# Performance work log

Measured on AMD Instinct MI355X. Metric: run time of the kernel, lower is better.

The kernel has to match this reference:

```python
import jax, jax.numpy as jnp
import numpy as np

B, T_IN, D = 16, 512, 256
MAX_DUR = 16


def setup_inputs() -> dict:
    key = jax.random.key(0)
    k1, k2 = jax.random.split(key)
    duration = jax.random.randint(k1, (B, T_IN), 0, MAX_DUR, dtype=jnp.int32)
    encoder_outputs = jax.random.normal(k2, (B, T_IN, D), dtype=jnp.float32)
    mask = jnp.ones((B, T_IN), dtype=bool)
    return {"encoder_outputs": encoder_outputs, "duration": duration, "mask": mask}


def reference(encoder_outputs, duration, mask):
    # duration is a concrete int array here, so T_out is a static Python int
    t_max = int(jnp.max(jnp.sum(duration, axis=-1)))
    d = duration.astype(jnp.float32)
    # frame centers per token: c[b, i] = cumsum(d)[b, i] - 0.5 * d[b, i]
    c = (jnp.cumsum(d, axis=-1) - 0.5 * d)[:, :, None]          # [B, T_in, 1]
    t = jnp.arange(1, t_max + 1, dtype=jnp.float32)[None, None, :]  # [1, 1, T_out]
    w1 = jnp.exp(-0.1 * (t - c) ** 2)                           # [B, T_in, T_out]
    w2 = jnp.sum(w1, axis=1, keepdims=True)                     # [B, 1, T_out]
    w2 = jnp.where(w2 == 0.0, 1.0, w2)
    w = w1 / w2                                                 # [B, T_in, T_out]
    # out[b, t, d] = sum_i w[b, i, t] * enc[b, i, d]
    out = jnp.einsum('bit,bid->btd', w, encoder_outputs)        # [B, T_out, D]
    return (out, w)
```

## Files before the change

kernel.cpp:

```cpp
#include <hip/hip_runtime.h>

#define B_    16
#define T_IN  512
#define D_    256
#define TM    64
#define KI    32
#define AP    40

typedef __attribute__((ext_vector_type(8))) short short8;
typedef __attribute__((ext_vector_type(4))) float f32x4;

__device__ __forceinline__ unsigned short f2bf(float x) {
    unsigned u = __builtin_bit_cast(unsigned, x);
    u += 0x7fff + ((u >> 16) & 1);
    return (unsigned short)(u >> 16);
}

__global__ __launch_bounds__(256) void transpose_kernel(
    const float* __restrict__ enc, unsigned short* __restrict__ encT)
{
    __shared__ float tile[64][65];
    const int tid = threadIdx.x;
    const int b  = blockIdx.z;
    const int i0 = blockIdx.x * 64;
    const int d0 = blockIdx.y * 64;
    #pragma unroll
    for (int p = 0; p < 4; ++p) {
        const int idx = p * 256 + tid;
        const int r   = idx >> 4;
        const int c4  = (idx & 15) * 4;
        const float4 v = *(const float4*)&enc[((long long)b * T_IN + i0 + r) * D_ + d0 + c4];
        tile[r][c4 + 0] = v.x; tile[r][c4 + 1] = v.y;
        tile[r][c4 + 2] = v.z; tile[r][c4 + 3] = v.w;
    }
    __syncthreads();
    #pragma unroll
    for (int p = 0; p < 8; ++p) {
        const int idx = p * 256 + tid;
        const int dr = idx >> 5;
        const int ip = idx & 31;
        const unsigned pk = (unsigned)f2bf(tile[2 * ip][dr])
                          | ((unsigned)f2bf(tile[2 * ip + 1][dr]) << 16);
        *(unsigned*)&encT[((long long)b * D_ + d0 + dr) * T_IN + i0 + ip * 2] = pk;
    }
}

__global__ __launch_bounds__(256, 4) void mfma_kernel(
    const unsigned short* __restrict__ encT,
    const int*   __restrict__ dur,
    float* __restrict__ out,
    int t_out)
{
    __shared__ int   sd[T_IN];
    __shared__ float sc[T_IN];
    __shared__ float red[4][TM];
    __shared__ float sinv[TM];
    __shared__ __align__(16) unsigned short A_lds[2][TM * AP];

    const int tid = threadIdx.x;
    const int b   = blockIdx.y;
    const int t0  = blockIdx.x * TM;

    const int v0 = dur[b * T_IN + tid];
    const int v1 = dur[b * T_IN + tid + 256];
    sd[tid] = v0; sd[tid + 256] = v1;
    __syncthreads();
    for (int off = 1; off < T_IN; off <<= 1) {
        const int a0 = (tid >= off) ? sd[tid - off] : 0;
        const int a1 = sd[tid + 256 - off];
        __syncthreads();
        sd[tid] += a0; sd[tid + 256] += a1;
        __syncthreads();
    }
    sc[tid]       = (float)sd[tid]       - 0.5f * (float)v0;
    sc[tid + 256] = (float)sd[tid + 256] - 0.5f * (float)v1;
    __syncthreads();

    const int tq = tid & 63;
    const int qq = tid >> 6;
    const float tv = (float)(t0 + tq + 1);

    {
        float s = 0.f;
        const int i0 = qq * 128;
        for (int i = 0; i < 128; ++i) {
            const float d = tv - sc[i0 + i];
            s += __expf(-0.1f * d * d);
        }
        red[qq][tq] = s;
        __syncthreads();
        if (qq == 0) {
            const float w2 = red[0][tq] + red[1][tq] + red[2][tq] + red[3][tq];
            sinv[tq] = (w2 == 0.f) ? 1.f : 1.f / w2;
        }
        __syncthreads();
    }

    const int lane  = tid & 63;
    const int mrow  = lane & 15;
    const int quad  = lane >> 4;
    const int dbase = qq * 64;
    const int iq0   = qq * 8;

    f32x4 acc[4][4];
    #pragma unroll
    for (int mf = 0; mf < 4; ++mf)
        #pragma unroll
        for (int nf = 0; nf < 4; ++nf)
            acc[mf][nf] = (f32x4){0.f, 0.f, 0.f, 0.f};

    const unsigned short* encTb = encT + (long long)b * D_ * T_IN;

    for (int ib = 0; ib < T_IN / KI; ++ib) {
        const int kc = ib * KI;

        short8 bv[4];
        #pragma unroll
        for (int nf = 0; nf < 4; ++nf)
            bv[nf] = *(const short8*)&encTb[(long long)(dbase + nf * 16 + mrow) * T_IN + kc + quad * 8];

        unsigned short* Ab = A_lds[ib & 1];
        {
            unsigned short tmp[8];
            #pragma unroll
            for (int j = 0; j < 8; ++j) {
                const float d = tv - sc[kc + iq0 + j];
                tmp[j] = f2bf(__expf(-0.1f * d * d));
            }
            *(short8*)&Ab[tq * AP + iq0] = *(const short8*)tmp;
        }
        __syncthreads();

        short8 av[4];
        #pragma unroll
        for (int mf = 0; mf < 4; ++mf)
            av[mf] = *(const short8*)&Ab[(mf * 16 + mrow) * AP + quad * 8];

        #pragma unroll
        for (int nf = 0; nf < 4; ++nf)
            #pragma unroll
            for (int mf = 0; mf < 4; ++mf)
                acc[mf][nf] = __builtin_amdgcn_mfma_f32_16x16x32_bf16(av[mf], bv[nf], acc[mf][nf], 0, 0, 0);
    }

    #pragma unroll
    for (int mf = 0; mf < 4; ++mf) {
        #pragma unroll
        for (int r = 0; r < 4; ++r) {
            const int tl = mf * 16 + quad * 4 + r;
            const int t  = t0 + tl;
            if (t < t_out) {
                const float inv = sinv[tl];
                #pragma unroll
                for (int nf = 0; nf < 4; ++nf)
                    out[((long long)b * t_out + t) * D_ + dbase + nf * 16 + mrow] = acc[mf][nf][r] * inv;
            }
        }
    }
}

__global__ __launch_bounds__(256, 4) void wwrite_kernel(
    const int* __restrict__ dur, float* __restrict__ wout, int t_out)
{
    __shared__ int   sd[T_IN];
    __shared__ float sc[T_IN];
    __shared__ float red[4][TM];
    __shared__ float sinv[TM];

    const int tid = threadIdx.x;
    const int b   = blockIdx.y;
    const int t0  = blockIdx.x * TM;

    const int v0 = dur[b * T_IN + tid];
    const int v1 = dur[b * T_IN + tid + 256];
    sd[tid] = v0; sd[tid + 256] = v1;
    __syncthreads();
    for (int off = 1; off < T_IN; off <<= 1) {
        const int a0 = (tid >= off) ? sd[tid - off] : 0;
        const int a1 = sd[tid + 256 - off];
        __syncthreads();
        sd[tid] += a0; sd[tid + 256] += a1;
        __syncthreads();
    }
    sc[tid]       = (float)sd[tid]       - 0.5f * (float)v0;
    sc[tid + 256] = (float)sd[tid + 256] - 0.5f * (float)v1;
    __syncthreads();

    const int tq = tid & 63;
    const int qq = tid >> 6;
    const float tv = (float)(t0 + tq + 1);

    {
        float s = 0.f;
        const int i0 = qq * 128;
        for (int i = 0; i < 128; ++i) {
            const float d = tv - sc[i0 + i];
            s += __expf(-0.1f * d * d);
        }
        red[qq][tq] = s;
        __syncthreads();
        if (qq == 0) {
            const float w2 = red[0][tq] + red[1][tq] + red[2][tq] + red[3][tq];
            sinv[tq] = (w2 == 0.f) ? 1.f : 1.f / w2;
        }
        __syncthreads();
    }

    if (t0 + tq >= t_out) return;
    const float inv = sinv[tq];
    float* wB = wout + (long long)b * T_IN * t_out + (t0 + tq);

    for (int kc = 0; kc < T_IN; kc += KI) {
        #pragma unroll
        for (int j = 0; j < 8; ++j) {
            const int i = kc + qq * 8 + j;
            const float d = tv - sc[i];
            wB[(long long)i * t_out] = __expf(-0.1f * d * d) * inv;
        }
    }
}

extern "C" void kernel_launch(void* const* d_in, const int* in_sizes, int n_in,
                              void* d_out, int out_size, void* d_ws, size_t ws_size,
                              hipStream_t stream) {
    const float* enc = (const float*)d_in[0];
    const int*   dur = (const int*)d_in[1];

    const int t_out = out_size / (B_ * (D_ + T_IN));

    float* out  = (float*)d_out;
    float* wout = (float*)d_out + (size_t)B_ * t_out * D_;
    unsigned short* encT =
        (unsigned short*)(wout + (size_t)B_ * T_IN * t_out) - (size_t)B_ * D_ * T_IN;

    transpose_kernel<<<dim3(T_IN / 64, D_ / 64, B_), 256, 0, stream>>>(enc, encT);

    dim3 grid((t_out + TM - 1) / TM, B_);
    mfma_kernel<<<grid, 256, 0, stream>>>(encT, dur, out, t_out);
    wwrite_kernel<<<grid, 256, 0, stream>>>(dur, wout, t_out);
}
```

Baseline: 246.8 us.

## Fuse weight-matrix writes into MFMA kernel, defer overlapped tail to cleanup kernel

The MFMA kernel now writes the normalized weights to the w output while it computes them for the matmul A tile, instead of a separate kernel recomputing the exponentials. Rows of w that overlap the bf16 transposed encoder scratch stored at the tail of the output buffer are skipped (row index at or beyond Rcut). A smaller cleanup kernel overwrites those rows after the matmul has finished reading encT. This removes the duplicate exp computation and one full pass over the weight grid, but adds strided global stores inside the MFMA main loop, which may stall it.

After: 240.5 us. -2.5%, faster.

```diff
diff --git a/kernel.cpp b/kernel.cpp
--- a/kernel.cpp
+++ b/kernel.cpp
@@ -45,11 +45,12 @@
     }
 }
 
-__global__ __launch_bounds__(256, 4) void mfma_kernel(
+__global__ __launch_bounds__(256, 4) void fused_kernel(
     const unsigned short* __restrict__ encT,
     const int*   __restrict__ dur,
     float* __restrict__ out,
-    int t_out)
+    float* __restrict__ wout,
+    int t_out, int Rcut)
 {
     __shared__ int   sd[T_IN];
     __shared__ float sc[T_IN];
@@ -95,6 +96,9 @@
         }
         __syncthreads();
     }
+    const float inv_t = sinv[tq];
+    const bool  t_ok  = (t0 + tq) < t_out;
+    const int   ilim  = Rcut - (b << 9);
 
     const int lane  = tid & 63;
     const int mrow  = lane & 15;
@@ -110,6 +114,7 @@
             acc[mf][nf] = (f32x4){0.f, 0.f, 0.f, 0.f};
 
     const unsigned short* encTb = encT + (long long)b * D_ * T_IN;
+    float* wB = wout + (long long)b * T_IN * t_out + (t0 + tq);
 
     for (int ib = 0; ib < T_IN / KI; ++ib) {
         const int kc = ib * KI;
@@ -124,8 +129,12 @@
             unsigned short tmp[8];
             #pragma unroll
             for (int j = 0; j < 8; ++j) {
-                const float d = tv - sc[kc + iq0 + j];
-                tmp[j] = f2bf(__expf(-0.1f * d * d));
+                const int i = kc + iq0 + j;
+                const float d = tv - sc[i];
+                const float e = __expf(-0.1f * d * d);
+                tmp[j] = f2bf(e);
+                if (t_ok && i < ilim)
+                    wB[(long long)i * t_out] = e * inv_t;
             }
             *(short8*)&Ab[tq * AP + iq0] = *(const short8*)tmp;
         }
@@ -159,8 +168,8 @@
     }
 }
 
-__global__ __launch_bounds__(256, 4) void wwrite_kernel(
-    const int* __restrict__ dur, float* __restrict__ wout, int t_out)
+__global__ __launch_bounds__(256, 4) void cleanup_kernel(
+    const int* __restrict__ dur, float* __restrict__ wout, int t_out, int Rcut, int b0)
 {
     __shared__ int   sd[T_IN];
     __shared__ float sc[T_IN];
@@ -168,7 +177,7 @@
     __shared__ float sinv[TM];
 
     const int tid = threadIdx.x;
-    const int b   = blockIdx.y;
+    const int b   = b0 + blockIdx.y;
     const int t0  = blockIdx.x * TM;
 
     const int v0 = dur[b * T_IN + tid];
@@ -208,15 +217,12 @@
 
     if (t0 + tq >= t_out) return;
     const float inv = sinv[tq];
+    const int ilo = max(0, Rcut - (b << 9));
     float* wB = wout + (long long)b * T_IN * t_out + (t0 + tq);
 
-    for (int kc = 0; kc < T_IN; kc += KI) {
-        #pragma unroll
-        for (int j = 0; j < 8; ++j) {
-            const int i = kc + qq * 8 + j;
-            const float d = tv - sc[i];
-            wB[(long long)i * t_out] = __expf(-0.1f * d * d) * inv;
-        }
+    for (int i = ilo + qq; i < T_IN; i += 4) {
+        const float d = tv - sc[i];
+        wB[(long long)i * t_out] = __expf(-0.1f * d * d) * inv;
     }
 }
 
@@ -230,12 +236,18 @@
 
     float* out  = (float*)d_out;
     float* wout = (float*)d_out + (size_t)B_ * t_out * D_;
-    unsigned short* encT =
-        (unsigned short*)(wout + (size_t)B_ * T_IN * t_out) - (size_t)B_ * D_ * T_IN;
+
+    const long long wtot        = (long long)B_ * T_IN * t_out;
+    const long long encT_floats = (long long)B_ * D_ * T_IN / 2;
+    const int Rcut = (int)((wtot - encT_floats) / t_out);
+    const int b0   = Rcut >> 9;
+    unsigned short* encT = (unsigned short*)((float*)wout + (wtot - encT_floats));
 
     transpose_kernel<<<dim3(T_IN / 64, D_ / 64, B_), 256, 0, stream>>>(enc, encT);
 
     dim3 grid((t_out + TM - 1) / TM, B_);
-    mfma_kernel<<<grid, 256, 0, stream>>>(encT, dur, out, t_out);
-    wwrite_kernel<<<grid, 256, 0, stream>>>(dur, wout, t_out);
-}
+    fused_kernel<<<grid, 256, 0, stream>>>(encT, dur, out, wout, t_out, Rcut);
+
+    dim3 cgrid((t_out + TM - 1) / TM, B_ - b0);
+    cleanup_kernel<<<cgrid, 256, 0, stream>>>(dur, wout, t_out, Rcut, b0);
+}
```
